# Kernel optimization log

Measured on AMD Instinct MI355X. Metric: run time of the kernel, lower is better.

Reference implementation:

```python
import jax, jax.numpy as jnp
import numpy as np

NA, NW = 131072, 131072
N = NA + NW
E = 1048576
R = 4
DIN = 64
H = 128
L = 2
EPS = 1e-5


def setup_inputs() -> dict:
    key = jax.random.key(0)
    ks = jax.random.split(key, 20)
    s_in = 1.0 / np.sqrt(DIN)
    s_h = 1.0 / np.sqrt(H)
    return {
        "x_assignments": jax.random.normal(ks[0], (NA, DIN), jnp.float32),
        "x_workers": jax.random.normal(ks[1], (NW, DIN), jnp.float32),
        "edge_index": jax.random.randint(ks[2], (2, E), 0, N),
        "edge_type": jax.random.randint(ks[3], (E,), 0, R),
        "W_in_a": jax.random.normal(ks[4], (DIN, H), jnp.float32) * s_in,
        "b_in_a": jnp.zeros((H,), jnp.float32),
        "W_in_w": jax.random.normal(ks[5], (DIN, H), jnp.float32) * s_in,
        "b_in_w": jnp.zeros((H,), jnp.float32),
        "W_rel": jax.random.normal(ks[6], (L, R, H, H), jnp.float32) * s_h,
        "W_root": jax.random.normal(ks[7], (L, H, H), jnp.float32) * s_h,
        "b_conv": jnp.zeros((L, H), jnp.float32),
        "ln_g": jnp.ones((L, H), jnp.float32),
        "ln_b": jnp.zeros((L, H), jnp.float32),
        "W_out": jax.random.normal(ks[8], (H, 1), jnp.float32) * s_h,
        "b_out": jnp.zeros((1,), jnp.float32),
        "base": jnp.zeros((), jnp.float32),
    }


def _layernorm(x, g, b):
    mu = jnp.mean(x, axis=-1, keepdims=True)
    var = jnp.var(x, axis=-1, keepdims=True)
    return (x - mu) * jax.lax.rsqrt(var + EPS) * g + b


def reference(x_assignments, x_workers, edge_index, edge_type,
              W_in_a, b_in_a, W_in_w, b_in_w,
              W_rel, W_root, b_conv, ln_g, ln_b,
              W_out, b_out, base):
    # type-specific input projection + relu, then flatten node space
    ha = jax.nn.relu(x_assignments @ W_in_a + b_in_a)
    hw = jax.nn.relu(x_workers @ W_in_w + b_in_w)
    h = jnp.concatenate([ha, hw], axis=0)  # [N, H]
    src, dst = edge_index[0], edge_index[1]
    for l in range(L):
        hs = h[src]  # [E, H] gathered source features
        out = h @ W_root[l] + b_conv[l]  # root transform + bias
        for r in range(R):
            m = (edge_type == r).astype(h.dtype)  # [E]
            agg = jax.ops.segment_sum(hs * m[:, None], dst, num_segments=N)
            cnt = jax.ops.segment_sum(m, dst, num_segments=N)
            mean = agg / jnp.maximum(cnt, 1.0)[:, None]  # per-relation mean aggr
            out = out + mean @ W_rel[l, r]
        h = jax.nn.relu(_layernorm(out, ln_g[l], ln_b[l]))
        # dropout inactive (eval mode)
    h_t = h[:NA]  # target node type slice (offset 0)
    pred = base + (h_t @ W_out + b_out)[:, 0]
    return pred
```

## Files before the change

### kernel.cpp

```cpp
#include <hip/hip_runtime.h>

#define NA_ 131072
#define NN  262144
#define EE  1048576
#define RR  4
#define EPS_ 1e-5f

typedef unsigned short ushort_t;
typedef unsigned char uchar_t;
typedef unsigned int uint_t;
typedef __attribute__((ext_vector_type(8))) short bf16x8;
typedef __attribute__((ext_vector_type(4))) float f32x4;

__device__ __forceinline__ float bf2f(uint_t u16) {
    return __uint_as_float(u16 << 16);
}
__device__ __forceinline__ uint_t f2bf(float f) {
    uint_t x = __float_as_uint(f);
    return (x + 0x7fffu + ((x >> 16) & 1u)) >> 16;
}

__device__ __forceinline__ void gl2lds16(const void* g, void* l) {
    __builtin_amdgcn_global_load_lds(
        (const __attribute__((address_space(1))) void*)g,
        (__attribute__((address_space(3))) void*)l, 16, 0, 0);
}

__global__ __launch_bounds__(256) void proj_gemm(const float* __restrict__ A,
                                                 const short* __restrict__ Btg,
                                                 const float* __restrict__ bias,
                                                 ushort_t* __restrict__ C) {
    const int K = 64;
    __shared__ short As[128][K + 8];
    __shared__ short Bs[128][K + 8];
    const int tid  = threadIdx.x;
    const int lane = tid & 63;
    const int l15  = lane & 15;
    const int q    = lane >> 4;
    const int wv   = tid >> 6;
    const int wr   = (wv >> 1) * 64;
    const int wc   = (wv & 1) * 64;
    const size_t blockRow = (size_t)blockIdx.x * 128;

    #pragma unroll
    for (int it = 0; it < 4; it++) {
        int sidx = (it * 256 + tid) * 8;
        int row = sidx / K, col = sidx % K;
        const float* Ag = A + (blockRow + row) * K + col;
        float4 v0 = *(const float4*)Ag;
        float4 v1 = *(const float4*)(Ag + 4);
        uint4 u;
        u.x = f2bf(v0.x) | (f2bf(v0.y) << 16);
        u.y = f2bf(v0.z) | (f2bf(v0.w) << 16);
        u.z = f2bf(v1.x) | (f2bf(v1.y) << 16);
        u.w = f2bf(v1.z) | (f2bf(v1.w) << 16);
        *(uint4*)&As[row][col] = u;
        *(uint4*)&Bs[row][col] = *(const uint4*)(Btg + (size_t)row * K + col);
    }
    __syncthreads();

    f32x4 acc[4][4];
    #pragma unroll
    for (int i = 0; i < 4; i++)
        #pragma unroll
        for (int j = 0; j < 4; j++) {
            acc[i][j][0] = 0.f; acc[i][j][1] = 0.f;
            acc[i][j][2] = 0.f; acc[i][j][3] = 0.f;
        }

    #pragma unroll
    for (int kk = 0; kk < 2; kk++) {
        bf16x8 af[4], bfr[4];
        #pragma unroll
        for (int i = 0; i < 4; i++)
            af[i] = *(const bf16x8*)&As[wr + i * 16 + l15][kk * 32 + q * 8];
        #pragma unroll
        for (int j = 0; j < 4; j++)
            bfr[j] = *(const bf16x8*)&Bs[wc + j * 16 + l15][kk * 32 + q * 8];
        #pragma unroll
        for (int i = 0; i < 4; i++)
            #pragma unroll
            for (int j = 0; j < 4; j++)
                acc[i][j] = __builtin_amdgcn_mfma_f32_16x16x32_bf16(
                    af[i], bfr[j], acc[i][j], 0, 0, 0);
    }

    #pragma unroll
    for (int j = 0; j < 4; j++) {
        int gcol = wc + j * 16 + l15;
        float bv = bias[gcol];
        #pragma unroll
        for (int i = 0; i < 4; i++) {
            size_t rbase = blockRow + wr + i * 16 + q * 4;
            #pragma unroll
            for (int r = 0; r < 4; r++) {
                float v = fmaxf(acc[i][j][r] + bv, 0.f);
                C[(rbase + r) * 128 + gcol] = (ushort_t)f2bf(v);
            }
        }
    }
}

__global__ void prep_weights(const float* __restrict__ Wia,
                             const float* __restrict__ Wiw,
                             const float* __restrict__ Wroot,
                             const float* __restrict__ Wrel,
                             short* __restrict__ wt) {
    int e = blockIdx.x * 256 + threadIdx.x;
    if (e < 8192) {
        int k = e >> 7, n = e & 127;
        wt[n * 64 + k] = (short)f2bf(Wia[e]);
    } else if (e < 16384) {
        int t = e - 8192;
        int k = t >> 7, n = t & 127;
        wt[8192 + n * 64 + k] = (short)f2bf(Wiw[t]);
    } else {
        int t = e - 16384;
        int l = t / 81920;
        int d = t % 81920;
        int kc = d / 16384;
        int rem2 = d % 16384;
        int n = rem2 >> 7;
        int kkk = rem2 & 127;
        float val = (kc < 4)
            ? Wrel[(((size_t)l * 4 + kc) * 128 + kkk) * 128 + n]
            : Wroot[((size_t)l * 128 + kkk) * 128 + n];
        wt[16384 + (size_t)l * 81920 + kc * 16384 + n * 128 + kkk] =
            (short)f2bf(val);
    }
}

__global__ void count_edges(const int* __restrict__ dstv,
                            const int* __restrict__ et,
                            uint_t* __restrict__ cntp,
                            uchar_t* __restrict__ rank) {
    int base = blockIdx.x * 1024 + threadIdx.x;
    int e0 = base, e1 = base + 256, e2 = base + 512, e3 = base + 768;
    int r0 = et[e0], r1 = et[e1], r2 = et[e2], r3 = et[e3];
    int d0 = dstv[e0], d1 = dstv[e1], d2 = dstv[e2], d3 = dstv[e3];
    uint_t o0 = atomicAdd(&cntp[d0], 1u << (8 * r0));
    uint_t o1 = atomicAdd(&cntp[d1], 1u << (8 * r1));
    uint_t o2 = atomicAdd(&cntp[d2], 1u << (8 * r2));
    uint_t o3 = atomicAdd(&cntp[d3], 1u << (8 * r3));
    rank[e0] = (uchar_t)((o0 >> (8 * r0)) & 0xffu);
    rank[e1] = (uchar_t)((o1 >> (8 * r1)) & 0xffu);
    rank[e2] = (uchar_t)((o2 >> (8 * r2)) & 0xffu);
    rank[e3] = (uchar_t)((o3 >> (8 * r3)) & 0xffu);
}

__global__ void inv_deg(uint_t* __restrict__ cntp, float* __restrict__ inv,
                        int* __restrict__ deg) {
    int i = blockIdx.x * 256 + threadIdx.x;
    if (i < NN) {
        uint_t c = cntp[i];
        int c0 = c & 255, c1 = (c >> 8) & 255, c2 = (c >> 16) & 255, c3 = c >> 24;
        float4 w;
        w.x = 1.0f / (float)(c0 > 1 ? c0 : 1);
        w.y = 1.0f / (float)(c1 > 1 ? c1 : 1);
        w.z = 1.0f / (float)(c2 > 1 ? c2 : 1);
        w.w = 1.0f / (float)(c3 > 1 ? c3 : 1);
        ((float4*)inv)[i] = w;
        deg[i] = c0 + c1 + c2 + c3;
        cntp[i] = ((uint_t)c0 << 8) | ((uint_t)(c0 + c1) << 16)
                | ((uint_t)(c0 + c1 + c2) << 24);
    }
}

__global__ void scan1(const int* __restrict__ deg, int* __restrict__ offs,
                      int* __restrict__ bsum) {
    __shared__ int lds[256];
    int tid = threadIdx.x;
    int i = blockIdx.x * 256 + tid;
    int v = deg[i];
    int incl = v;
    lds[tid] = incl;
    __syncthreads();
    for (int off = 1; off < 256; off <<= 1) {
        int t = (tid >= off) ? lds[tid - off] : 0;
        __syncthreads();
        incl += t;
        lds[tid] = incl;
        __syncthreads();
    }
    offs[i] = incl - v;
    if (tid == 255) bsum[blockIdx.x] = incl;
}

__global__ void scan_bsum(int* __restrict__ bsum) {
    __shared__ int lds[256];
    int tid = threadIdx.x;
    int t0 = bsum[tid * 4 + 0], t1 = bsum[tid * 4 + 1];
    int t2 = bsum[tid * 4 + 2], t3 = bsum[tid * 4 + 3];
    int s = t0 + t1 + t2 + t3;
    int incl = s;
    lds[tid] = incl;
    __syncthreads();
    for (int off = 1; off < 256; off <<= 1) {
        int t = (tid >= off) ? lds[tid - off] : 0;
        __syncthreads();
        incl += t;
        lds[tid] = incl;
        __syncthreads();
    }
    int e = incl - s;
    bsum[tid * 4 + 0] = e;
    bsum[tid * 4 + 1] = e + t0;
    bsum[tid * 4 + 2] = e + t0 + t1;
    bsum[tid * 4 + 3] = e + t0 + t1 + t2;
}

__global__ void scan_add(int* __restrict__ offs, const int* __restrict__ bsum) {
    int i = blockIdx.x * 256 + threadIdx.x;
    offs[i] = offs[i] + bsum[blockIdx.x];
    if (i == 0) offs[NN] = EE;
}

__global__ void place_edges(const int* __restrict__ srcv,
                            const int* __restrict__ dstv,
                            const int* __restrict__ et,
                            const uchar_t* __restrict__ rank,
                            const int* __restrict__ offs,
                            const uint_t* __restrict__ pref,
                            uint_t* __restrict__ pk) {
    int base = blockIdx.x * 1024 + threadIdx.x;
    #pragma unroll
    for (int t = 0; t < 4; t++) {
        int e = base + t * 256;
        int d = dstv[e], r = et[e];
        int pos = offs[d] + (int)((pref[d] >> (8 * r)) & 255u) + (int)rank[e];
        pk[pos] = (uint_t)srcv[e] | ((uint_t)r << 18);
    }
}

__global__ __launch_bounds__(256) void agg_means(const uint_t* __restrict__ pk,
                                                 const int* __restrict__ offs,
                                                 const ushort_t* __restrict__ hold,
                                                 const float* __restrict__ inv,
                                                 ushort_t* __restrict__ M,
                                                 int lo, int rowsCap) {
    const int wv  = __builtin_amdgcn_readfirstlane(threadIdx.x >> 6);
    const int idx = blockIdx.x * 4 + wv;
    const int d   = lo + idx;
    const int lane = threadIdx.x & 63;
    const int beg = offs[d];
    const int end = offs[d + 1];
    const float4 w4 = ((const float4*)inv)[d];

    float a0x = 0.f, a0y = 0.f, a1x = 0.f, a1y = 0.f;
    float a2x = 0.f, a2y = 0.f, a3x = 0.f, a3y = 0.f;

    const uint_t* hold32 = (const uint_t*)hold;

    auto accs = [&](uint_t p, uint_t v, bool valid) {
        float x = bf2f(v & 0xffffu), y = bf2f(v >> 16);
        uint_t r = p >> 18;
        float m0 = (valid && r == 0u) ? 1.f : 0.f;
        float m1 = (valid && r == 1u) ? 1.f : 0.f;
        float m2 = (valid && r == 2u) ? 1.f : 0.f;
        float m3 = (valid && r == 3u) ? 1.f : 0.f;
        a0x += m0 * x;  a0y += m0 * y;
        a1x += m1 * x;  a1y += m1 * y;
        a2x += m2 * x;  a2y += m2 * y;
        a3x += m3 * x;  a3y += m3 * y;
    };

    for (int e = beg; e < end; e += 8) {
        const int last = end - 1;
        int a1i = (e + 1 < end) ? e + 1 : last;
        int a2i = (e + 2 < end) ? e + 2 : last;
        int a3i = (e + 3 < end) ? e + 3 : last;
        uint_t p0 = pk[e];
        uint_t p1 = pk[a1i];
        uint_t p2 = pk[a2i];
        uint_t p3 = pk[a3i];
        uint_t v0 = hold32[(size_t)(p0 & 0x3FFFFu) * 64 + lane];
        uint_t v1 = hold32[(size_t)(p1 & 0x3FFFFu) * 64 + lane];
        uint_t v2 = hold32[(size_t)(p2 & 0x3FFFFu) * 64 + lane];
        uint_t v3 = hold32[(size_t)(p3 & 0x3FFFFu) * 64 + lane];

        const bool hB = (e + 4 < end);
        if (hB) {
            int b1i = (e + 5 < end) ? e + 5 : last;
            int b2i = (e + 6 < end) ? e + 6 : last;
            int b3i = (e + 7 < end) ? e + 7 : last;
            uint_t q0 = pk[e + 4];
            uint_t q1 = pk[b1i];
            uint_t q2 = pk[b2i];
            uint_t q3 = pk[b3i];
            uint_t u0 = hold32[(size_t)(q0 & 0x3FFFFu) * 64 + lane];
            uint_t u1 = hold32[(size_t)(q1 & 0x3FFFFu) * 64 + lane];
            uint_t u2 = hold32[(size_t)(q2 & 0x3FFFFu) * 64 + lane];
            uint_t u3 = hold32[(size_t)(q3 & 0x3FFFFu) * 64 + lane];
            accs(p0, v0, true);
            accs(p1, v1, true);
            accs(p2, v2, true);
            accs(p3, v3, true);
            accs(q0, u0, true);
            accs(q1, u1, e + 5 < end);
            accs(q2, u2, e + 6 < end);
            accs(q3, u3, e + 7 < end);
        } else {
            accs(p0, v0, true);
            accs(p1, v1, e + 1 < end);
            accs(p2, v2, e + 2 < end);
            accs(p3, v3, e + 3 < end);
        }
    }

    uint_t* P = (uint_t*)M;
    size_t planeU = (size_t)rowsCap * 64;
    size_t rowU = (size_t)idx * 64 + lane;
    P[rowU]              = f2bf(a0x * w4.x) | (f2bf(a0y * w4.x) << 16);
    P[planeU + rowU]     = f2bf(a1x * w4.y) | (f2bf(a1y * w4.y) << 16);
    P[2 * planeU + rowU] = f2bf(a2x * w4.z) | (f2bf(a2y * w4.z) << 16);
    P[3 * planeU + rowU] = f2bf(a3x * w4.w) | (f2bf(a3y * w4.w) << 16);
}

template<bool HEAD>
__global__ __launch_bounds__(256) void layer_gemm_ln(
    const ushort_t* __restrict__ Mg,
    const ushort_t* __restrict__ hold,
    const short* __restrict__ Btg,
    const float* __restrict__ bconv,
    const float* __restrict__ lng,
    const float* __restrict__ lnb,
    ushort_t* __restrict__ hnew,
    const float* __restrict__ Wout,
    const float* __restrict__ bout,
    const float* __restrict__ basep,
    float* __restrict__ pred,
    int lo, int rowsCap) {
    __shared__ short As[64 * 128];
    __shared__ short Bs[128 * 128];
    __shared__ float lds_s[64][2], lds_q[64][2], lds_h[64][2];

    const int tid  = threadIdx.x;
    const int lane = tid & 63;
    const int l15  = lane & 15;
    const int q    = lane >> 4;
    const int wv   = tid >> 6;
    const int wr   = (wv >> 1) * 32;
    const int wc   = (wv & 1) * 64;
    const int blockRowL = blockIdx.x * 64;
    const size_t planeS = (size_t)rowsCap * 128;

    f32x4 acc[2][4];
    #pragma unroll
    for (int i = 0; i < 2; i++)
        #pragma unroll
        for (int j = 0; j < 4; j++) {
            acc[i][j][0] = 0.f; acc[i][j][1] = 0.f;
            acc[i][j][2] = 0.f; acc[i][j][3] = 0.f;
        }

    const int rloc = lane >> 4;
    const int gsw  = (lane & 15) ^ ((wv * 4 + rloc) & 15);
    const int lby  = (rloc << 8) + (gsw << 4);

    for (int kc = 0; kc < 5; kc++) {
        const char* asrc = (kc < 4)
            ? (const char*)(Mg + (size_t)kc * planeS + (size_t)blockRowL * 128)
            : (const char*)(hold + (size_t)(lo + blockRowL) * 128);
        const char* bsrc = (const char*)(Btg + (size_t)kc * 16384);
        __syncthreads();
        #pragma unroll
        for (int it = 0; it < 8; it++) {
            int off = it * 4096 + wv * 1024;
            if (it < 4) gl2lds16(asrc + off + lby, (char*)As + off);
            gl2lds16(bsrc + off + lby, (char*)Bs + off);
        }
        __syncthreads();

        #pragma unroll
        for (int kk = 0; kk < 4; kk++) {
            bf16x8 af[2], bfr[4];
            #pragma unroll
            for (int i = 0; i < 2; i++)
                af[i] = *(const bf16x8*)
                    &As[(wr + i * 16 + l15) * 128 + (((kk * 4 + q) ^ l15) << 3)];
            #pragma unroll
            for (int j = 0; j < 4; j++)
                bfr[j] = *(const bf16x8*)
                    &Bs[(wc + j * 16 + l15) * 128 + (((kk * 4 + q) ^ l15) << 3)];
            #pragma unroll
            for (int i = 0; i < 2; i++)
                #pragma unroll
                for (int j = 0; j < 4; j++)
                    acc[i][j] = __builtin_amdgcn_mfma_f32_16x16x32_bf16(
                        af[i], bfr[j], acc[i][j], 0, 0, 0);
        }
    }

    float bj[4], gj[4], bbj[4], wj[4];
    #pragma unroll
    for (int j = 0; j < 4; j++) {
        int col = wc + j * 16 + l15;
        bj[j]  = bconv[col];
        gj[j]  = lng[col];
        bbj[j] = lnb[col];
        if (HEAD) wj[j] = Wout[col];
    }
    #pragma unroll
    for (int i = 0; i < 2; i++)
        #pragma unroll
        for (int j = 0; j < 4; j++)
            #pragma unroll
            for (int r = 0; r < 4; r++) acc[i][j][r] += bj[j];

    float ps[2][4], pq[2][4];
    #pragma unroll
    for (int i = 0; i < 2; i++)
        #pragma unroll
        for (int r = 0; r < 4; r++) {
            float s = 0.f, qq = 0.f;
            #pragma unroll
            for (int j = 0; j < 4; j++) {
                float v = acc[i][j][r];
                s += v;
                qq += v * v;
            }
            ps[i][r] = s;
            pq[i][r] = qq;
        }
    #pragma unroll
    for (int m = 1; m <= 8; m <<= 1)
        #pragma unroll
        for (int i = 0; i < 2; i++)
            #pragma unroll
            for (int r = 0; r < 4; r++) {
                ps[i][r] += __shfl_xor(ps[i][r], m);
                pq[i][r] += __shfl_xor(pq[i][r], m);
            }

    if (l15 == 0) {
        #pragma unroll
        for (int i = 0; i < 2; i++)
            #pragma unroll
            for (int r = 0; r < 4; r++) {
                int row = wr + i * 16 + q * 4 + r;
                lds_s[row][wv & 1] = ps[i][r];
                lds_q[row][wv & 1] = pq[i][r];
            }
    }
    __syncthreads();

    float hs[2][4];
    #pragma unroll
    for (int i = 0; i < 2; i++)
        #pragma unroll
        for (int r = 0; r < 4; r++) {
            int row = wr + i * 16 + q * 4 + r;
            float sum = lds_s[row][0] + lds_s[row][1];
            float sq  = lds_q[row][0] + lds_q[row][1];
            float mu  = sum * (1.0f / 128.0f);
            float var = sq * (1.0f / 128.0f) - mu * mu;
            float rs  = rsqrtf(var + EPS_);
            size_t gr = (size_t)(lo + blockRowL + row) * 128;
            float hd = 0.f;
            #pragma unroll
            for (int j = 0; j < 4; j++) {
                float v = (acc[i][j][r] - mu) * rs * gj[j] + bbj[j];
                v = fmaxf(v, 0.f);
                if (HEAD) hd += v * wj[j];
                else hnew[gr + wc + j * 16 + l15] = (ushort_t)f2bf(v);
            }
            if (HEAD) hs[i][r] = hd;
        }

    if (HEAD) {
        #pragma unroll
        for (int m = 1; m <= 8; m <<= 1)
            #pragma unroll
            for (int i = 0; i < 2; i++)
                #pragma unroll
                for (int r = 0; r < 4; r++)
                    hs[i][r] += __shfl_xor(hs[i][r], m);
        if (l15 == 0) {
            #pragma unroll
            for (int i = 0; i < 2; i++)
                #pragma unroll
                for (int r = 0; r < 4; r++) {
                    int row = wr + i * 16 + q * 4 + r;
                    lds_h[row][wv & 1] = hs[i][r];
                }
        }
        __syncthreads();
        if (tid < 64)
            pred[lo + blockRowL + tid] =
                lds_h[tid][0] + lds_h[tid][1] + bout[0] + basep[0];
    }
}

extern "C" void kernel_launch(void* const* d_in, const int* in_sizes, int n_in,
                              void* d_out, int out_size, void* d_ws, size_t ws_size,
                              hipStream_t stream) {
    const float* x_a    = (const float*)d_in[0];
    const float* x_w    = (const float*)d_in[1];
    const int*   eidx   = (const int*)d_in[2];
    const int*   etype  = (const int*)d_in[3];
    const float* W_in_a = (const float*)d_in[4];
    const float* b_in_a = (const float*)d_in[5];
    const float* W_in_w = (const float*)d_in[6];
    const float* b_in_w = (const float*)d_in[7];
    const float* W_rel  = (const float*)d_in[8];
    const float* W_root = (const float*)d_in[9];
    const float* b_conv = (const float*)d_in[10];
    const float* ln_g   = (const float*)d_in[11];
    const float* ln_b   = (const float*)d_in[12];
    const float* W_out  = (const float*)d_in[13];
    const float* b_out  = (const float*)d_in[14];
    const float* base   = (const float*)d_in[15];

    const int* src  = eidx;
    const int* dstv = eidx + EE;

    char* p = (char*)d_ws;
    auto alloc = [&](size_t bytes) {
        char* q = p;
        p += (bytes + 255) & ~(size_t)255;
        return q;
    };
    ushort_t* hB   = (ushort_t*)alloc((size_t)NN * 128 * 2);
    float*    inv  = (float*)alloc((size_t)RR * NN * 4);
    uint_t*   pk   = (uint_t*)alloc((size_t)EE * 4);
    int*      offs = (int*)alloc((size_t)(NN + 1) * 4);
    short*    wbuf = (short*)alloc((size_t)180224 * 2);
    char*     hA_region = p;
    ushort_t* hA   = (ushort_t*)alloc((size_t)NN * 128 * 2);
    char*     scratch = p;
    uint_t*   cntp = (uint_t*)alloc((size_t)NN * 4);
    uchar_t*  rank = (uchar_t*)alloc((size_t)EE);
    int*      deg  = (int*)alloc((size_t)NN * 4);
    int*      bsum = (int*)alloc((size_t)1024 * 4);

    size_t rem0 = (ws_size > (size_t)(scratch - (char*)d_ws))
                      ? (ws_size - (size_t)(scratch - (char*)d_ws)) : 0;
    int cap0 = (int)(rem0 / 1024);
    if (cap0 > NN) cap0 = NN;
    cap0 &= ~127;
    if (cap0 == 0) cap0 = 128;
    size_t rem1 = (ws_size > (size_t)(hA_region - (char*)d_ws))
                      ? (ws_size - (size_t)(hA_region - (char*)d_ws)) : 0;
    int cap1 = (int)(rem1 / 1024);
    if (cap1 > NA_) cap1 = NA_;
    cap1 &= ~127;
    if (cap1 == 0) cap1 = 128;

    short* wt_ina = wbuf;
    short* wt_inw = wbuf + 8192;
    auto wt_layer = [&](int l) { return wbuf + 16384 + (size_t)l * 81920; };

    hipMemsetAsync(cntp, 0, (size_t)NN * sizeof(uint_t), stream);
    count_edges<<<EE / 1024, 256, 0, stream>>>(dstv, etype, cntp, rank);
    inv_deg<<<NN / 256, 256, 0, stream>>>(cntp, inv, deg);
    scan1<<<NN / 256, 256, 0, stream>>>(deg, offs, bsum);
    scan_bsum<<<1, 256, 0, stream>>>(bsum);
    scan_add<<<NN / 256, 256, 0, stream>>>(offs, bsum);
    place_edges<<<EE / 1024, 256, 0, stream>>>(src, dstv, etype, rank, offs,
                                               cntp, pk);

    prep_weights<<<704, 256, 0, stream>>>(W_in_a, W_in_w, W_root, W_rel, wbuf);

    proj_gemm<<<NA_ / 128, 256, 0, stream>>>(x_a, wt_ina, b_in_a, hA);
    proj_gemm<<<NA_ / 128, 256, 0, stream>>>(x_w, wt_inw, b_in_w,
                                             hA + (size_t)NA_ * 128);

    ushort_t* hc = hA;
    ushort_t* hn = hB;
    for (int l = 0; l < 2; l++) {
        int Nout = (l == 0) ? NN : NA_;
        ushort_t* M = (l == 0) ? (ushort_t*)scratch : (ushort_t*)hA_region;
        int cap = (l == 0) ? cap0 : cap1;
        int nch = (Nout + cap - 1) / cap;
        int chunk = ((Nout / nch) + 127) & ~127;
        if (chunk > cap) chunk = cap;
        for (int lo = 0; lo < Nout; lo += chunk) {
            int cr = (Nout - lo < chunk) ? (Nout - lo) : chunk;
            agg_means<<<cr / 4, 256, 0, stream>>>(pk, offs, hc, inv, M, lo,
                                                  cap);
            if (l == 0)
                layer_gemm_ln<false><<<cr / 64, 256, 0, stream>>>(
                    M, hc, wt_layer(l), b_conv + l * 128, ln_g + l * 128,
                    ln_b + l * 128, hn, nullptr, nullptr, nullptr, nullptr,
                    lo, cap);
            else
                layer_gemm_ln<true><<<cr / 64, 256, 0, stream>>>(
                    M, hc, wt_layer(l), b_conv + l * 128, ln_g + l * 128,
                    ln_b + l * 128, nullptr, W_out, b_out, base,
                    (float*)d_out, lo, cap);
        }
        ushort_t* t = hc; hc = hn; hn = t;
    }
}
```

Measured before the change: 501.2 us.

## Pad edge counters to cache lines and use nontemporal mean stores/loads

```diff
diff --git a/kernel.cpp b/kernel.cpp
--- a/kernel.cpp
+++ b/kernel.cpp
@@ -24,6 +24,11 @@
     __builtin_amdgcn_global_load_lds(
         (const __attribute__((address_space(1))) void*)g,
         (__attribute__((address_space(3))) void*)l, 16, 0, 0);
+}
+__device__ __forceinline__ void gl2lds16_nt(const void* g, void* l) {
+    __builtin_amdgcn_global_load_lds(
+        (const __attribute__((address_space(1))) void*)g,
+        (__attribute__((address_space(3))) void*)l, 16, 0, 2);
 }
 
 __global__ __launch_bounds__(256) void proj_gemm(const float* __restrict__ A,
@@ -138,21 +143,23 @@
     int e0 = base, e1 = base + 256, e2 = base + 512, e3 = base + 768;
     int r0 = et[e0], r1 = et[e1], r2 = et[e2], r3 = et[e3];
     int d0 = dstv[e0], d1 = dstv[e1], d2 = dstv[e2], d3 = dstv[e3];
-    uint_t o0 = atomicAdd(&cntp[d0], 1u << (8 * r0));
-    uint_t o1 = atomicAdd(&cntp[d1], 1u << (8 * r1));
-    uint_t o2 = atomicAdd(&cntp[d2], 1u << (8 * r2));
-    uint_t o3 = atomicAdd(&cntp[d3], 1u << (8 * r3));
+    uint_t o0 = atomicAdd(&cntp[(size_t)d0 * 16], 1u << (8 * r0));
+    uint_t o1 = atomicAdd(&cntp[(size_t)d1 * 16], 1u << (8 * r1));
+    uint_t o2 = atomicAdd(&cntp[(size_t)d2 * 16], 1u << (8 * r2));
+    uint_t o3 = atomicAdd(&cntp[(size_t)d3 * 16], 1u << (8 * r3));
     rank[e0] = (uchar_t)((o0 >> (8 * r0)) & 0xffu);
     rank[e1] = (uchar_t)((o1 >> (8 * r1)) & 0xffu);
     rank[e2] = (uchar_t)((o2 >> (8 * r2)) & 0xffu);
     rank[e3] = (uchar_t)((o3 >> (8 * r3)) & 0xffu);
 }
 
-__global__ void inv_deg(uint_t* __restrict__ cntp, float* __restrict__ inv,
-                        int* __restrict__ deg) {
+__global__ void inv_deg(const uint_t* __restrict__ cntp,
+                        float* __restrict__ inv,
+                        int* __restrict__ deg,
+                        uint_t* __restrict__ prefd) {
     int i = blockIdx.x * 256 + threadIdx.x;
     if (i < NN) {
-        uint_t c = cntp[i];
+        uint_t c = cntp[(size_t)i * 16];
         int c0 = c & 255, c1 = (c >> 8) & 255, c2 = (c >> 16) & 255, c3 = c >> 24;
         float4 w;
         w.x = 1.0f / (float)(c0 > 1 ? c0 : 1);
@@ -161,8 +168,8 @@
         w.w = 1.0f / (float)(c3 > 1 ? c3 : 1);
         ((float4*)inv)[i] = w;
         deg[i] = c0 + c1 + c2 + c3;
-        cntp[i] = ((uint_t)c0 << 8) | ((uint_t)(c0 + c1) << 16)
-                | ((uint_t)(c0 + c1 + c2) << 24);
+        prefd[i] = ((uint_t)c0 << 8) | ((uint_t)(c0 + c1) << 16)
+                 | ((uint_t)(c0 + c1 + c2) << 24);
     }
 }
 
@@ -220,14 +227,14 @@
                             const int* __restrict__ et,
                             const uchar_t* __restrict__ rank,
                             const int* __restrict__ offs,
-                            const uint_t* __restrict__ pref,
+                            const uint_t* __restrict__ prefd,
                             uint_t* __restrict__ pk) {
     int base = blockIdx.x * 1024 + threadIdx.x;
     #pragma unroll
     for (int t = 0; t < 4; t++) {
         int e = base + t * 256;
         int d = dstv[e], r = et[e];
-        int pos = offs[d] + (int)((pref[d] >> (8 * r)) & 255u) + (int)rank[e];
+        int pos = offs[d] + (int)((prefd[d] >> (8 * r)) & 255u) + (int)rank[e];
         pk[pos] = (uint_t)srcv[e] | ((uint_t)r << 18);
     }
 }
@@ -310,10 +317,14 @@
     uint_t* P = (uint_t*)M;
     size_t planeU = (size_t)rowsCap * 64;
     size_t rowU = (size_t)idx * 64 + lane;
-    P[rowU]              = f2bf(a0x * w4.x) | (f2bf(a0y * w4.x) << 16);
-    P[planeU + rowU]     = f2bf(a1x * w4.y) | (f2bf(a1y * w4.y) << 16);
-    P[2 * planeU + rowU] = f2bf(a2x * w4.z) | (f2bf(a2y * w4.z) << 16);
-    P[3 * planeU + rowU] = f2bf(a3x * w4.w) | (f2bf(a3y * w4.w) << 16);
+    __builtin_nontemporal_store(
+        f2bf(a0x * w4.x) | (f2bf(a0y * w4.x) << 16), &P[rowU]);
+    __builtin_nontemporal_store(
+        f2bf(a1x * w4.y) | (f2bf(a1y * w4.y) << 16), &P[planeU + rowU]);
+    __builtin_nontemporal_store(
+        f2bf(a2x * w4.z) | (f2bf(a2y * w4.z) << 16), &P[2 * planeU + rowU]);
+    __builtin_nontemporal_store(
+        f2bf(a3x * w4.w) | (f2bf(a3y * w4.w) << 16), &P[3 * planeU + rowU]);
 }
 
 template<bool HEAD>
@@ -366,7 +377,10 @@
         #pragma unroll
         for (int it = 0; it < 8; it++) {
             int off = it * 4096 + wv * 1024;
-            if (it < 4) gl2lds16(asrc + off + lby, (char*)As + off);
+            if (it < 4) {
+                if (kc < 4) gl2lds16_nt(asrc + off + lby, (char*)As + off);
+                else        gl2lds16(asrc + off + lby, (char*)As + off);
+            }
             gl2lds16(bsrc + off + lby, (char*)Bs + off);
         }
         __syncthreads();
@@ -528,10 +542,11 @@
     char*     hA_region = p;
     ushort_t* hA   = (ushort_t*)alloc((size_t)NN * 128 * 2);
     char*     scratch = p;
-    uint_t*   cntp = (uint_t*)alloc((size_t)NN * 4);
-    uchar_t*  rank = (uchar_t*)alloc((size_t)EE);
-    int*      deg  = (int*)alloc((size_t)NN * 4);
-    int*      bsum = (int*)alloc((size_t)1024 * 4);
+    uint_t*   cntp  = (uint_t*)alloc((size_t)NN * 64);
+    uchar_t*  rank  = (uchar_t*)alloc((size_t)EE);
+    int*      deg   = (int*)alloc((size_t)NN * 4);
+    uint_t*   prefd = (uint_t*)alloc((size_t)NN * 4);
+    int*      bsum  = (int*)alloc((size_t)1024 * 4);
 
     size_t rem0 = (ws_size > (size_t)(scratch - (char*)d_ws))
                       ? (ws_size - (size_t)(scratch - (char*)d_ws)) : 0;
@@ -550,14 +565,14 @@
     short* wt_inw = wbuf + 8192;
     auto wt_layer = [&](int l) { return wbuf + 16384 + (size_t)l * 81920; };
 
-    hipMemsetAsync(cntp, 0, (size_t)NN * sizeof(uint_t), stream);
+    hipMemsetAsync(cntp, 0, (size_t)NN * 64, stream);
     count_edges<<<EE / 1024, 256, 0, stream>>>(dstv, etype, cntp, rank);
-    inv_deg<<<NN / 256, 256, 0, stream>>>(cntp, inv, deg);
+    inv_deg<<<NN / 256, 256, 0, stream>>>(cntp, inv, deg, prefd);
     scan1<<<NN / 256, 256, 0, stream>>>(deg, offs, bsum);
     scan_bsum<<<1, 256, 0, stream>>>(bsum);
     scan_add<<<NN / 256, 256, 0, stream>>>(offs, bsum);
     place_edges<<<EE / 1024, 256, 0, stream>>>(src, dstv, etype, rank, offs,
-                                               cntp, pk);
+                                               prefd, pk);
 
     prep_weights<<<704, 256, 0, stream>>>(W_in_a, W_in_w, W_root, W_rel, wbuf);
 
```

New measurement: 507.6 us. No clear change (+1.3%).
